# Kernel optimization log

Hardware: AMD Instinct MI355X
Metric: run time of the kernel (lower is better)

## Reference

```python
import jax, jax.numpy as jnp
import numpy as np

B, N, RIN, ROUT, DEMB, FIN, FE, E, ITERS = 64, 128, 32, 64, 64, 64, 16, 65536, 3
NTOT = B * N


def gnn(x, edge_index, edge_feat, Ws, Wm, We, b):
    # edge-conditioned message passing: [NTOT, Fin] -> [NTOT, Fout]
    src, dst = edge_index[0], edge_index[1]
    msg = jax.nn.relu(x[src] @ Wm + edge_feat @ We)          # [E, Fout]
    agg = jax.ops.segment_sum(msg, dst, num_segments=x.shape[0])
    return jax.nn.relu(x @ Ws + agg + b)


def setup_inputs() -> dict:
    key = jax.random.key(0)
    ks = jax.random.split(key, 20)
    s = 0.1
    return {
        "x_r": jax.random.normal(ks[0], (NTOT, FIN), jnp.float32),
        "edge_index_r": jax.random.randint(ks[1], (2, E), 0, NTOT),
        "edge_feat_r": jax.random.normal(ks[2], (E, FE), jnp.float32),
        "x_p": jax.random.normal(ks[3], (NTOT, FIN), jnp.float32),
        "edge_index_p": jax.random.randint(ks[4], (2, E), 0, NTOT),
        "edge_feat_p": jax.random.normal(ks[5], (E, FE), jnp.float32),
        "r_mask": jnp.ones((B, N), dtype=bool),
        "p_mask": jnp.ones((B, N), dtype=bool),
        # gnn_1 params (FIN -> DEMB)
        "g1_Ws": jax.random.normal(ks[6], (FIN, DEMB)) * s,
        "g1_Wm": jax.random.normal(ks[7], (FIN, DEMB)) * s,
        "g1_We": jax.random.normal(ks[8], (FE, DEMB)) * s,
        "g1_b": jnp.zeros((DEMB,), jnp.float32),
        # gnn_2 params (RIN -> ROUT)
        "g2_Ws": jax.random.normal(ks[9], (RIN, ROUT)) * s,
        "g2_Wm": jax.random.normal(ks[10], (RIN, ROUT)) * s,
        "g2_We": jax.random.normal(ks[11], (FE, ROUT)) * s,
        "g2_b": jnp.zeros((ROUT,), jnp.float32),
        # consensus mlp (ROUT -> ROUT -> 1)
        "mlp_W1": jax.random.normal(ks[12], (ROUT, ROUT)) * s,
        "mlp_b1": jnp.zeros((ROUT,), jnp.float32),
        "mlp_W2": jax.random.normal(ks[13], (ROUT, 1)) * s,
        "mlp_b2": jnp.zeros((1,), jnp.float32),
    }


def reference(x_r, edge_index_r, edge_feat_r, x_p, edge_index_p, edge_feat_p,
              r_mask, p_mask,
              g1_Ws, g1_Wm, g1_We, g1_b,
              g2_Ws, g2_Wm, g2_We, g2_b,
              mlp_W1, mlp_b1, mlp_W2, mlp_b2):
    # node embeddings via gnn_1, then dense-batch to [B, N, DEMB]
    h_r = gnn(x_r, edge_index_r, edge_feat_r, g1_Ws, g1_Wm, g1_We, g1_b).reshape(B, N, DEMB)
    h_p = gnn(x_p, edge_index_p, edge_feat_p, g1_Ws, g1_Wm, g1_We, g1_b).reshape(B, N, DEMB)

    M_hat = jnp.einsum('brd,bpd->brp', h_r, h_p)             # [B, N_r, N_p]
    M_mask = r_mask[:, :, None] & p_mask[:, None, :]
    M_0 = jax.nn.softmax(M_hat, axis=-1).reshape(NTOT, N)    # packed (full mask)

    rkey = jax.random.key(42)
    for it in range(ITERS):
        M = jax.nn.softmax(M_hat, axis=-1)
        rf_r = jax.random.normal(jax.random.fold_in(rkey, it), (B, N, RIN), jnp.float32)
        rf_p = jnp.einsum('brp,bri->bpi', M, rf_r)           # M^T @ rand
        o_r = gnn(rf_r.reshape(NTOT, RIN), edge_index_r, edge_feat_r,
                  g2_Ws, g2_Wm, g2_We, g2_b).reshape(B, N, ROUT)
        o_p = gnn(rf_p.reshape(NTOT, RIN), edge_index_p, edge_feat_p,
                  g2_Ws, g2_Wm, g2_We, g2_b).reshape(B, N, ROUT)
        D = o_r[:, :, None, :] - o_p[:, None, :, :]          # [B, N_r, N_p, ROUT]
        upd = (jax.nn.relu(D @ mlp_W1 + mlp_b1) @ mlp_W2 + mlp_b2)[..., 0]
        M_hat = M_hat + jnp.where(M_mask, upd, 0.0)

    M_T = jax.nn.softmax(M_hat, axis=-1).reshape(NTOT, N)
    return (M_0, M_T)
```

## Files before the change

kernel.cpp:

```cpp
#include <hip/hip_runtime.h>

constexpr int kE = 65536, kNTOT = 8192;

__host__ __device__ __forceinline__ void tf_round(unsigned& x0, unsigned& x1, int r) {
  x0 += x1;
  x1 = (x1 << r) | (x1 >> (32 - r));
  x1 ^= x0;
}
__host__ __device__ __forceinline__ void tf2x32(unsigned k0, unsigned k1,
                                                unsigned& x0, unsigned& x1) {
  unsigned ks2 = k0 ^ k1 ^ 0x1BD11BDAu;
  x0 += k0; x1 += k1;
  tf_round(x0,x1,13); tf_round(x0,x1,15); tf_round(x0,x1,26); tf_round(x0,x1,6);
  x0 += k1; x1 += ks2 + 1u;
  tf_round(x0,x1,17); tf_round(x0,x1,29); tf_round(x0,x1,16); tf_round(x0,x1,24);
  x0 += ks2; x1 += k0 + 2u;
  tf_round(x0,x1,13); tf_round(x0,x1,15); tf_round(x0,x1,26); tf_round(x0,x1,6);
  x0 += k0; x1 += k1 + 3u;
  tf_round(x0,x1,17); tf_round(x0,x1,29); tf_round(x0,x1,16); tf_round(x0,x1,24);
  x0 += k1; x1 += ks2 + 4u;
  tf_round(x0,x1,13); tf_round(x0,x1,15); tf_round(x0,x1,26); tf_round(x0,x1,6);
  x0 += ks2; x1 += k0 + 5u;
}

__device__ __forceinline__ float bits_to_normal(unsigned bits) {
  float f = __uint_as_float((bits >> 9) | 0x3f800000u) - 1.0f;
  const float LO = -0.99999994f;
  float u = fmaf(f, 2.0f, LO);
  u = fmaxf(u, LO);
  float w = -log1pf(-u * u);
  float p;
  if (w < 5.0f) {
    w -= 2.5f;
    p = 2.81022636e-08f;
    p = fmaf(p, w, 3.43273939e-07f);
    p = fmaf(p, w, -3.5233877e-06f);
    p = fmaf(p, w, -4.39150654e-06f);
    p = fmaf(p, w, 0.00021858087f);
    p = fmaf(p, w, -0.00125372503f);
    p = fmaf(p, w, -0.00417768164f);
    p = fmaf(p, w, 0.246640727f);
    p = fmaf(p, w, 1.50140941f);
  } else {
    w = sqrtf(w) - 3.0f;
    p = -0.000200214257f;
    p = fmaf(p, w, 0.000100950558f);
    p = fmaf(p, w, 0.00134934322f);
    p = fmaf(p, w, -0.00367342844f);
    p = fmaf(p, w, 0.00573950773f);
    p = fmaf(p, w, -0.0076224613f);
    p = fmaf(p, w, 0.00943887047f);
    p = fmaf(p, w, 1.00167406f);
    p = fmaf(p, w, 2.83297682f);
  }
  return 1.41421356f * (p * u);
}

__device__ __forceinline__ float redmax32(float v) {
#pragma unroll
  for (int o = 16; o > 0; o >>= 1) v = fmaxf(v, __shfl_xor(v, o));
  return v;
}
__device__ __forceinline__ float redsum32(float v) {
#pragma unroll
  for (int o = 16; o > 0; o >>= 1) v += __shfl_xor(v, o);
  return v;
}

__global__ __launch_bounds__(256) void hist_kern(const int* __restrict__ eiR,
                                                 const int* __restrict__ eiP,
                                                 int* __restrict__ offR,
                                                 int* __restrict__ offP,
                                                 float* __restrict__ aggz,
                                                 float* __restrict__ rfpz) {
  int i = blockIdx.x * 256 + threadIdx.x;
  float4 z4 = make_float4(0.f, 0.f, 0.f, 0.f);
  float4* z = reinterpret_cast<float4*>(aggz) + i * 2;
  z[0] = z4; z[1] = z4;
  reinterpret_cast<float2*>(rfpz)[i] = make_float2(0.f, 0.f);
  const int* ei = (i < kE) ? eiR : eiP;
  int* off = (i < kE) ? offR : offP;
  int e = i & (kE - 1);
  atomicAdd(&off[ei[kE + e]], 1);
}

__global__ __launch_bounds__(512) void scan_kern(int* __restrict__ offR,
                                                 int* __restrict__ offP) {
  int* off = blockIdx.x ? offP : offR;
  int t = threadIdx.x;
  int base = t * 16;
  int v[16];
#pragma unroll
  for (int i = 0; i < 16; ++i) v[i] = off[base + i];
  int sum = 0;
#pragma unroll
  for (int i = 0; i < 16; ++i) sum += v[i];
  int lane = t & 63, w = t >> 6;
  int incl = sum;
#pragma unroll
  for (int o = 1; o < 64; o <<= 1) {
    int y = __shfl_up(incl, o);
    if (lane >= o) incl += y;
  }
  __shared__ int wsum[8];
  if (lane == 63) wsum[w] = incl;
  __syncthreads();
  int woff = 0;
#pragma unroll
  for (int i = 0; i < 8; ++i) if (i < w) woff += wsum[i];
  int running = woff + incl - sum;
#pragma unroll
  for (int i = 0; i < 16; ++i) {
    off[base + i] = running;
    running += v[i];
  }
}

__global__ __launch_bounds__(256) void scatter_kern(
    const int* __restrict__ eiR, const int* __restrict__ eiP,
    int* __restrict__ offR, int* __restrict__ offP,
    int4* __restrict__ ebR, int4* __restrict__ ebP) {
  int i = blockIdx.x * 256 + threadIdx.x;
  const int* ei = (i < kE) ? eiR : eiP;
  int* off = (i < kE) ? offR : offP;
  int4* eb = (i < kE) ? ebR : ebP;
  int e = i & (kE - 1);
  int src = ei[e];
  int dst = ei[kE + e];
  int pos = atomicAdd(&off[dst], 1);
  eb[pos] = make_int4(src, e, dst, 0);
}

__global__ __launch_bounds__(512) void xw_gemm64(
    const float* __restrict__ inR, const float* __restrict__ inP,
    float* __restrict__ xwR, float* __restrict__ xwP,
    const float* __restrict__ W) {
  __shared__ float sX[64][68];
  __shared__ float sW[64][68];
  bool isP = blockIdx.x >= 128;
  const float* in = isP ? inP : inR;
  float* xw = isP ? xwP : xwR;
  int n0 = (blockIdx.x & 127) * 64;
  int t = threadIdx.x;
#pragma unroll
  for (int idx = 0; idx < 2; ++idx) {
    int q = t * 4 + idx * 2048;
    int k = q >> 6, j = q & 63;
    *reinterpret_cast<float4*>(&sW[k][j]) = *reinterpret_cast<const float4*>(W + q);
    float4 v = *reinterpret_cast<const float4*>(in + (size_t)n0 * 64 + q);
    sX[j + 0][k] = v.x; sX[j + 1][k] = v.y; sX[j + 2][k] = v.z; sX[j + 3][k] = v.w;
  }
  __syncthreads();
  int tn = (t & 31) * 2, tj = (t >> 5) * 4;
  float acc[2][4] = {};
#pragma unroll 8
  for (int k = 0; k < 64; ++k) {
    float2 a = *reinterpret_cast<const float2*>(&sX[k][tn]);
    float4 b = *reinterpret_cast<const float4*>(&sW[k][tj]);
    acc[0][0] = fmaf(a.x, b.x, acc[0][0]); acc[0][1] = fmaf(a.x, b.y, acc[0][1]);
    acc[0][2] = fmaf(a.x, b.z, acc[0][2]); acc[0][3] = fmaf(a.x, b.w, acc[0][3]);
    acc[1][0] = fmaf(a.y, b.x, acc[1][0]); acc[1][1] = fmaf(a.y, b.y, acc[1][1]);
    acc[1][2] = fmaf(a.y, b.z, acc[1][2]); acc[1][3] = fmaf(a.y, b.w, acc[1][3]);
  }
#pragma unroll
  for (int i = 0; i < 2; ++i) {
    *reinterpret_cast<float4*>(&xw[(size_t)(n0 + tn + i) * 64 + tj]) =
        make_float4(acc[i][0], acc[i][1], acc[i][2], acc[i][3]);
  }
}

__global__ __launch_bounds__(512) void xwp_gemm(
    const float* __restrict__ rfp, float* __restrict__ xwP,
    const float* __restrict__ W) {
  __shared__ float sX[32][68];
  __shared__ float sW[32][68];
  int n0 = blockIdx.x * 64;
  int t = threadIdx.x;
  {
    int q = t * 4;
    *reinterpret_cast<float4*>(&sW[q >> 6][q & 63]) = *reinterpret_cast<const float4*>(W + q);
    int r = q >> 5, kk = q & 31;
    float4 v = *reinterpret_cast<const float4*>(rfp + (size_t)n0 * 32 + q);
    sX[kk][r] = v.x; sX[kk + 1][r] = v.y; sX[kk + 2][r] = v.z; sX[kk + 3][r] = v.w;
  }
  __syncthreads();
  int tn = (t & 31) * 2, tj = (t >> 5) * 4;
  float acc[2][4] = {};
#pragma unroll 8
  for (int k = 0; k < 32; ++k) {
    float2 a = *reinterpret_cast<const float2*>(&sX[k][tn]);
    float4 b = *reinterpret_cast<const float4*>(&sW[k][tj]);
    acc[0][0] = fmaf(a.x, b.x, acc[0][0]); acc[0][1] = fmaf(a.x, b.y, acc[0][1]);
    acc[0][2] = fmaf(a.x, b.z, acc[0][2]); acc[0][3] = fmaf(a.x, b.w, acc[0][3]);
    acc[1][0] = fmaf(a.y, b.x, acc[1][0]); acc[1][1] = fmaf(a.y, b.y, acc[1][1]);
    acc[1][2] = fmaf(a.y, b.z, acc[1][2]); acc[1][3] = fmaf(a.y, b.w, acc[1][3]);
  }
#pragma unroll
  for (int i = 0; i < 2; ++i) {
    *reinterpret_cast<float4*>(&xwP[(size_t)(n0 + tn + i) * 64 + tj]) =
        make_float4(acc[i][0], acc[i][1], acc[i][2], acc[i][3]);
  }
}

__global__ __launch_bounds__(256) void msg_edge(
    const float* __restrict__ xwR, const float* __restrict__ efR,
    const int4* __restrict__ ebR, float* __restrict__ aggR,
    const float* __restrict__ xwP, const float* __restrict__ efP,
    const int4* __restrict__ ebP, float* __restrict__ aggP,
    const float* __restrict__ We) {
  __shared__ float sEF[16][68];
  __shared__ float sW[16][68];
  __shared__ float sOut[64][68];
  __shared__ int sDst[64];
  __shared__ int sSrc[64];
  __shared__ int sPerm[64];
  bool isP = blockIdx.x >= 1024;
  const float* xw = isP ? xwP : xwR;
  const float* ef = isP ? efP : efR;
  const int4* eb = isP ? ebP : ebR;
  float* agg = isP ? aggP : aggR;
  int i0 = (blockIdx.x & 1023) * 64;
  int t = threadIdx.x;
  {
    int q = t * 4;
    int k = q >> 6, j = q & 63;
    *reinterpret_cast<float4*>(&sW[k][j]) = *reinterpret_cast<const float4*>(We + q);
  }
  if (t < 64) {
    int4 er = eb[i0 + t];
    sSrc[t] = er.x;
    sPerm[t] = er.y;
    sDst[t] = er.z;
  }
  __syncthreads();
  {
    int l = t & 3;
    int g = t >> 2;
    int rb = g >> 2;
    int kq = g & 3;
    int gbase = (t & 63) & ~3;
    int k4 = kq * 4;
    int r = rb * 4 + l;
    const float* rptr = ef + (size_t)sPerm[r] * 16 + k4;
    float4 v = *reinterpret_cast<const float4*>(rptr);
    float vc[4] = {v.x, v.y, v.z, v.w};
    float out[4];
#pragma unroll
    for (int c = 0; c < 4; ++c) {
      float val = vc[(l - c) & 3];
      out[(l + c) & 3] = __shfl(val, gbase + ((l + c) & 3), 64);
    }
    *reinterpret_cast<float4*>(&sEF[k4 + l][rb * 4]) =
        make_float4(out[0], out[1], out[2], out[3]);
  }
  __syncthreads();
  int tn = (t & 15) * 4, tj = (t >> 4) * 4;
  float acc[4][4] = {};
#pragma unroll
  for (int k = 0; k < 16; ++k) {
    float4 a = *reinterpret_cast<const float4*>(&sEF[k][tn]);
    float4 b = *reinterpret_cast<const float4*>(&sW[k][tj]);
    acc[0][0] = fmaf(a.x, b.x, acc[0][0]); acc[0][1] = fmaf(a.x, b.y, acc[0][1]);
    acc[0][2] = fmaf(a.x, b.z, acc[0][2]); acc[0][3] = fmaf(a.x, b.w, acc[0][3]);
    acc[1][0] = fmaf(a.y, b.x, acc[1][0]); acc[1][1] = fmaf(a.y, b.y, acc[1][1]);
    acc[1][2] = fmaf(a.y, b.z, acc[1][2]); acc[1][3] = fmaf(a.y, b.w, acc[1][3]);
    acc[2][0] = fmaf(a.z, b.x, acc[2][0]); acc[2][1] = fmaf(a.z, b.y, acc[2][1]);
    acc[2][2] = fmaf(a.z, b.z, acc[2][2]); acc[2][3] = fmaf(a.z, b.w, acc[2][3]);
    acc[3][0] = fmaf(a.w, b.x, acc[3][0]); acc[3][1] = fmaf(a.w, b.y, acc[3][1]);
    acc[3][2] = fmaf(a.w, b.z, acc[3][2]); acc[3][3] = fmaf(a.w, b.w, acc[3][3]);
  }
#pragma unroll
  for (int i = 0; i < 4; ++i) {
    float4 g = *reinterpret_cast<const float4*>(xw + (size_t)sSrc[tn + i] * 64 + tj);
    *reinterpret_cast<float4*>(&sOut[tn + i][tj]) =
        make_float4(fmaxf(acc[i][0] + g.x, 0.f), fmaxf(acc[i][1] + g.y, 0.f),
                    fmaxf(acc[i][2] + g.z, 0.f), fmaxf(acc[i][3] + g.w, 0.f));
  }
  __syncthreads();
  int col = t & 63;
  int r0l = (t >> 6) * 16;
  float run = 0.f;
  int rd = sDst[r0l];
#pragma unroll
  for (int r = 0; r < 16; ++r) {
    int d = sDst[r0l + r];
    if (d != rd) {
      unsafeAtomicAdd(&agg[(size_t)rd * 64 + col], run);
      run = 0.f; rd = d;
    }
    run += sOut[r0l + r][col];
  }
  unsafeAtomicAdd(&agg[(size_t)rd * 64 + col], run);
}

__global__ __launch_bounds__(512) void node1_gemm(
    const float* __restrict__ xR, float* __restrict__ aggR, float* __restrict__ hR,
    const float* __restrict__ xP, float* __restrict__ aggP, float* __restrict__ hP,
    const float* __restrict__ Ws, const float* __restrict__ bias) {
  __shared__ float sX[64][68];
  __shared__ float sW[64][68];
  bool isP = blockIdx.x >= 128;
  const float* x = isP ? xP : xR;
  float* agg = isP ? aggP : aggR;
  float* h = isP ? hP : hR;
  int n0 = (blockIdx.x & 127) * 64;
  int t = threadIdx.x;
#pragma unroll
  for (int idx = 0; idx < 2; ++idx) {
    int q = t * 4 + idx * 2048;
    int k = q >> 6, j = q & 63;
    *reinterpret_cast<float4*>(&sW[k][j]) = *reinterpret_cast<const float4*>(Ws + q);
    float4 v = *reinterpret_cast<const float4*>(x + (size_t)n0 * 64 + q);
    sX[j + 0][k] = v.x; sX[j + 1][k] = v.y; sX[j + 2][k] = v.z; sX[j + 3][k] = v.w;
  }
  __syncthreads();
  int tn = (t & 31) * 2, tj = (t >> 5) * 4;
  float acc[2][4] = {};
#pragma unroll 8
  for (int k = 0; k < 64; ++k) {
    float2 a = *reinterpret_cast<const float2*>(&sX[k][tn]);
    float4 b = *reinterpret_cast<const float4*>(&sW[k][tj]);
    acc[0][0] = fmaf(a.x, b.x, acc[0][0]); acc[0][1] = fmaf(a.x, b.y, acc[0][1]);
    acc[0][2] = fmaf(a.x, b.z, acc[0][2]); acc[0][3] = fmaf(a.x, b.w, acc[0][3]);
    acc[1][0] = fmaf(a.y, b.x, acc[1][0]); acc[1][1] = fmaf(a.y, b.y, acc[1][1]);
    acc[1][2] = fmaf(a.y, b.z, acc[1][2]); acc[1][3] = fmaf(a.y, b.w, acc[1][3]);
  }
  float4 bv = *reinterpret_cast<const float4*>(bias + tj);
  float4 z4 = make_float4(0.f, 0.f, 0.f, 0.f);
#pragma unroll
  for (int i = 0; i < 2; ++i) {
    int n = n0 + tn + i;
    float4 g = *reinterpret_cast<const float4*>(&agg[(size_t)n * 64 + tj]);
    *reinterpret_cast<float4*>(&agg[(size_t)n * 64 + tj]) = z4;
    float4 o;
    o.x = fmaxf(acc[i][0] + g.x + bv.x, 0.f);
    o.y = fmaxf(acc[i][1] + g.y + bv.y, 0.f);
    o.z = fmaxf(acc[i][2] + g.z + bv.z, 0.f);
    o.w = fmaxf(acc[i][3] + g.w + bv.w, 0.f);
    *reinterpret_cast<float4*>(&h[(size_t)n * 64 + tj]) = o;
  }
}

__device__ __forceinline__ void rfp_partial(const float sm[16][128],
                                            const float rfb[16][32],
                                            float* __restrict__ rfpB, int t) {
  float rfc[16];
  int iw = t & 31;
#pragma unroll
  for (int r = 0; r < 16; ++r) rfc[r] = rfb[r][iw];
#pragma unroll
  for (int rep = 0; rep < 16; ++rep) {
    int p = rep * 8 + (t >> 5);
    float a = 0.f;
#pragma unroll
    for (int r = 0; r < 16; ++r) a = fmaf(sm[r][p], rfc[r], a);
    unsafeAtomicAdd(&rfpB[p * 32 + iw], a);
  }
}

__device__ __forceinline__ void gen_rfr_tile(float* __restrict__ rfr,
                                             float rfb[16][32], int b, int r0,
                                             int t, unsigned fk0, unsigned fk1) {
  unsigned base = (unsigned)((b * 128 + r0) * 32);
#pragma unroll
  for (int q = 0; q < 2; ++q) {
    unsigned j = (unsigned)(q * 256 + t);
    unsigned i = base + j;
    unsigned a0 = 0u, a1 = i;
    tf2x32(fk0, fk1, a0, a1);
    float v = bits_to_normal(a0 ^ a1);
    rfr[i] = v;
    rfb[j >> 5][j & 31] = v;
  }
}

__device__ __forceinline__ void xwr_direct(const float rfb[16][32],
                                           const float* __restrict__ Wm2,
                                           float* __restrict__ xwR,
                                           int b, int r0, int t) {
  int rl = t >> 4, c0 = (t & 15) * 4;
  float4 a = make_float4(0.f, 0.f, 0.f, 0.f);
#pragma unroll 8
  for (int k = 0; k < 32; ++k) {
    float rv = rfb[rl][k];
    float4 w = *reinterpret_cast<const float4*>(Wm2 + k * 64 + c0);
    a.x = fmaf(rv, w.x, a.x); a.y = fmaf(rv, w.y, a.y);
    a.z = fmaf(rv, w.z, a.z); a.w = fmaf(rv, w.w, a.w);
  }
  *reinterpret_cast<float4*>(&xwR[(size_t)(b * 128 + r0 + rl) * 64 + c0]) = a;
}

__global__ __launch_bounds__(256) void mhat_soft(
    const float* __restrict__ hR, const float* __restrict__ hP,
    float* __restrict__ Mhat, float* __restrict__ M0out,
    float* __restrict__ rfr, float* __restrict__ rfp,
    float* __restrict__ xwR, const float* __restrict__ Wm2,
    unsigned fk0, unsigned fk1) {
  __shared__ float hr[16][66];
  __shared__ float hp[128][66];
  __shared__ float sm[16][128];
  __shared__ float rfb[16][32];
  int gid = blockIdx.x, t = threadIdx.x;
  int b = gid >> 3, r0 = (gid & 7) * 16;
  gen_rfr_tile(rfr, rfb, b, r0, t, fk0, fk1);
  const float* hrG = hR + ((size_t)(b * 128 + r0)) * 64;
  {
    int q = t * 4; int r = q >> 6, d = q & 63;
    float4 v = *reinterpret_cast<const float4*>(hrG + q);
    hr[r][d] = v.x; hr[r][d + 1] = v.y; hr[r][d + 2] = v.z; hr[r][d + 3] = v.w;
  }
  const float* hpG = hP + (size_t)b * 128 * 64;
#pragma unroll
  for (int rep = 0; rep < 8; ++rep) {
    int q = (rep * 256 + t) * 4; int p = q >> 6, d = q & 63;
    float4 v = *reinterpret_cast<const float4*>(hpG + q);
    hp[p][d] = v.x; hp[p][d + 1] = v.y; hp[p][d + 2] = v.z; hp[p][d + 3] = v.w;
  }
  __syncthreads();
  xwr_direct(rfb, Wm2, xwR, b, r0, t);
  int tx = t & 31, ty = t >> 5;
  float acc[2][4] = {};
  for (int d = 0; d < 64; ++d) {
    float a0 = hr[ty][d], a1 = hr[ty + 8][d];
    float q0 = hp[tx][d], q1 = hp[tx + 32][d], q2 = hp[tx + 64][d], q3 = hp[tx + 96][d];
    acc[0][0] = fmaf(a0, q0, acc[0][0]); acc[0][1] = fmaf(a0, q1, acc[0][1]);
    acc[0][2] = fmaf(a0, q2, acc[0][2]); acc[0][3] = fmaf(a0, q3, acc[0][3]);
    acc[1][0] = fmaf(a1, q0, acc[1][0]); acc[1][1] = fmaf(a1, q1, acc[1][1]);
    acc[1][2] = fmaf(a1, q2, acc[1][2]); acc[1][3] = fmaf(a1, q3, acc[1][3]);
  }
#pragma unroll
  for (int ii = 0; ii < 2; ++ii) {
    int r = r0 + ty + 8 * ii;
    float* mrow = Mhat + ((size_t)(b * 128 + r)) * 128;
    mrow[tx] = acc[ii][0]; mrow[tx + 32] = acc[ii][1];
    mrow[tx + 64] = acc[ii][2]; mrow[tx + 96] = acc[ii][3];
    float mx = redmax32(fmaxf(fmaxf(acc[ii][0], acc[ii][1]), fmaxf(acc[ii][2], acc[ii][3])));
    float e0 = __expf(acc[ii][0] - mx), e1 = __expf(acc[ii][1] - mx);
    float e2 = __expf(acc[ii][2] - mx), e3 = __expf(acc[ii][3] - mx);
    float inv = 1.0f / redsum32(e0 + e1 + e2 + e3);
    float* orow = M0out + ((size_t)(b * 128 + r)) * 128;
    orow[tx] = e0 * inv; orow[tx + 32] = e1 * inv;
    orow[tx + 64] = e2 * inv; orow[tx + 96] = e3 * inv;
    int rl = ty + 8 * ii;
    sm[rl][tx] = e0 * inv; sm[rl][tx + 32] = e1 * inv;
    sm[rl][tx + 64] = e2 * inv; sm[rl][tx + 96] = e3 * inv;
  }
  __syncthreads();
  rfp_partial(sm, rfb, rfp + (size_t)b * 4096, t);
}

__global__ __launch_bounds__(512) void node2u_gemm(
    const float* __restrict__ rfR, float* __restrict__ aggR, float* __restrict__ uR,
    const float* __restrict__ rfP, float* __restrict__ aggP, float* __restrict__ uP,
    const float* __restrict__ Ws2, const float* __restrict__ g2b,
    const float* __restrict__ W1, const float* __restrict__ b1,
    float* __restrict__ rfp_clear) {
  __shared__ float sRF[32][68];
  __shared__ float sW2[32][68];
  __shared__ float sW1[64][68];
  __shared__ float sO[64][68];
  bool isP = blockIdx.x >= 128;
  const float* rf = isP ? rfP : rfR;
  float* agg = isP ? aggP : aggR;
  float* u = isP ? uP : uR;
  int n0 = (blockIdx.x & 127) * 64;
  int t = threadIdx.x;
#pragma unroll
  for (int idx = 0; idx < 2; ++idx) {
    int q = t * 4 + idx * 2048;
    *reinterpret_cast<float4*>(&sW1[q >> 6][q & 63]) = *reinterpret_cast<const float4*>(W1 + q);
  }
  {
    int q = t * 4;
    *reinterpret_cast<float4*>(&sW2[q >> 6][q & 63]) = *reinterpret_cast<const float4*>(Ws2 + q);
    int r = q >> 5, kk = q & 31;
    float4 v = *reinterpret_cast<const float4*>(rf + (size_t)(n0 + r) * 32 + kk);
    sRF[kk][r] = v.x; sRF[kk + 1][r] = v.y; sRF[kk + 2][r] = v.z; sRF[kk + 3][r] = v.w;
  }
  __syncthreads();
  if (isP) {
    float4 z4 = make_float4(0.f, 0.f, 0.f, 0.f);
    reinterpret_cast<float4*>(rfp_clear + (size_t)n0 * 32)[t] = z4;
  }
  int tn = (t & 31) * 2, tj = (t >> 5) * 4;
  float acc[2][4] = {};
#pragma unroll 8
  for (int k = 0; k < 32; ++k) {
    float2 a = *reinterpret_cast<const float2*>(&sRF[k][tn]);
    float4 b = *reinterpret_cast<const float4*>(&sW2[k][tj]);
    acc[0][0] = fmaf(a.x, b.x, acc[0][0]); acc[0][1] = fmaf(a.x, b.y, acc[0][1]);
    acc[0][2] = fmaf(a.x, b.z, acc[0][2]); acc[0][3] = fmaf(a.x, b.w, acc[0][3]);
    acc[1][0] = fmaf(a.y, b.x, acc[1][0]); acc[1][1] = fmaf(a.y, b.y, acc[1][1]);
    acc[1][2] = fmaf(a.y, b.z, acc[1][2]); acc[1][3] = fmaf(a.y, b.w, acc[1][3]);
  }
  float4 bg = *reinterpret_cast<const float4*>(g2b + tj);
  float4 z4 = make_float4(0.f, 0.f, 0.f, 0.f);
#pragma unroll
  for (int i = 0; i < 2; ++i) {
    int n = n0 + tn + i;
    float4 g = *reinterpret_cast<const float4*>(&agg[(size_t)n * 64 + tj]);
    *reinterpret_cast<float4*>(&agg[(size_t)n * 64 + tj]) = z4;
    sO[tj + 0][tn + i] = fmaxf(acc[i][0] + g.x + bg.x, 0.f);
    sO[tj + 1][tn + i] = fmaxf(acc[i][1] + g.y + bg.y, 0.f);
    sO[tj + 2][tn + i] = fmaxf(acc[i][2] + g.z + bg.z, 0.f);
    sO[tj + 3][tn + i] = fmaxf(acc[i][3] + g.w + bg.w, 0.f);
  }
  __syncthreads();
  float acc2[2][4] = {};
#pragma unroll 8
  for (int k = 0; k < 64; ++k) {
    float2 a = *reinterpret_cast<const float2*>(&sO[k][tn]);
    float4 b = *reinterpret_cast<const float4*>(&sW1[k][tj]);
    acc2[0][0] = fmaf(a.x, b.x, acc2[0][0]); acc2[0][1] = fmaf(a.x, b.y, acc2[0][1]);
    acc2[0][2] = fmaf(a.x, b.z, acc2[0][2]); acc2[0][3] = fmaf(a.x, b.w, acc2[0][3]);
    acc2[1][0] = fmaf(a.y, b.x, acc2[1][0]); acc2[1][1] = fmaf(a.y, b.y, acc2[1][1]);
    acc2[1][2] = fmaf(a.y, b.z, acc2[1][2]); acc2[1][3] = fmaf(a.y, b.w, acc2[1][3]);
  }
  float4 b1v = make_float4(0.f, 0.f, 0.f, 0.f);
  if (!isP) b1v = *reinterpret_cast<const float4*>(b1 + tj);
#pragma unroll
  for (int i = 0; i < 2; ++i) {
    int n = n0 + tn + i;
    float4 o;
    o.x = acc2[i][0] + b1v.x; o.y = acc2[i][1] + b1v.y;
    o.z = acc2[i][2] + b1v.z; o.w = acc2[i][3] + b1v.w;
    *reinterpret_cast<float4*>(&u[(size_t)n * 64 + tj]) = o;
  }
}

__global__ __launch_bounds__(256) void upd_soft(
    const float* __restrict__ uR, const float* __restrict__ uP,
    const float* __restrict__ W2, const float* __restrict__ b2p,
    float* __restrict__ Mhat, float* __restrict__ outLast, int last,
    float* __restrict__ rfr, float* __restrict__ rfp,
    float* __restrict__ xwR, const float* __restrict__ Wm2,
    unsigned fk0, unsigned fk1) {
  __shared__ float sur[16][66];
  __shared__ float sup[128][66];
  __shared__ float sw2[64];
  __shared__ float sm[16][128];
  __shared__ float rfb[16][32];
  int gid = blockIdx.x, t = threadIdx.x;
  int b = gid >> 3, r0 = (gid & 7) * 16;
  if (!last) gen_rfr_tile(rfr, rfb, b, r0, t, fk0, fk1);
  const float* urG = uR + ((size_t)(b * 128 + r0)) * 64;
  {
    int q = t * 4; int r = q >> 6, d = q & 63;
    float4 v = *reinterpret_cast<const float4*>(urG + q);
    sur[r][d] = v.x; sur[r][d + 1] = v.y; sur[r][d + 2] = v.z; sur[r][d + 3] = v.w;
  }
  const float* upG = uP + (size_t)b * 128 * 64;
#pragma unroll
  for (int rep = 0; rep < 8; ++rep) {
    int q = (rep * 256 + t) * 4; int p = q >> 6, d = q & 63;
    float4 v = *reinterpret_cast<const float4*>(upG + q);
    sup[p][d] = v.x; sup[p][d + 1] = v.y; sup[p][d + 2] = v.z; sup[p][d + 3] = v.w;
  }
  if (t < 64) sw2[t] = W2[t];
  __syncthreads();
  if (!last) xwr_direct(rfb, Wm2, xwR, b, r0, t);
  int tx = t & 31, ty = t >> 5;
  float acc[2][4] = {};
  for (int j = 0; j < 64; ++j) {
    float w2v = sw2[j];
    float a0 = sur[ty][j], a1 = sur[ty + 8][j];
    float q0 = sup[tx][j], q1 = sup[tx + 32][j], q2 = sup[tx + 64][j], q3 = sup[tx + 96][j];
    acc[0][0] = fmaf(fmaxf(a0 - q0, 0.f), w2v, acc[0][0]);
    acc[0][1] = fmaf(fmaxf(a0 - q1, 0.f), w2v, acc[0][1]);
    acc[0][2] = fmaf(fmaxf(a0 - q2, 0.f), w2v, acc[0][2]);
    acc[0][3] = fmaf(fmaxf(a0 - q3, 0.f), w2v, acc[0][3]);
    acc[1][0] = fmaf(fmaxf(a1 - q0, 0.f), w2v, acc[1][0]);
    acc[1][1] = fmaf(fmaxf(a1 - q1, 0.f), w2v, acc[1][1]);
    acc[1][2] = fmaf(fmaxf(a1 - q2, 0.f), w2v, acc[1][2]);
    acc[1][3] = fmaf(fmaxf(a1 - q3, 0.f), w2v, acc[1][3]);
  }
  float b2v = b2p[0];
#pragma unroll
  for (int ii = 0; ii < 2; ++ii) {
    int r = r0 + ty + 8 * ii;
    float* mrow = Mhat + ((size_t)(b * 128 + r)) * 128;
    float m0 = mrow[tx] + acc[ii][0] + b2v;
    float m1 = mrow[tx + 32] + acc[ii][1] + b2v;
    float m2 = mrow[tx + 64] + acc[ii][2] + b2v;
    float m3 = mrow[tx + 96] + acc[ii][3] + b2v;
    if (!last) {
      mrow[tx] = m0; mrow[tx + 32] = m1; mrow[tx + 64] = m2; mrow[tx + 96] = m3;
    }
    float mx = redmax32(fmaxf(fmaxf(m0, m1), fmaxf(m2, m3)));
    float e0 = __expf(m0 - mx), e1 = __expf(m1 - mx);
    float e2 = __expf(m2 - mx), e3 = __expf(m3 - mx);
    float inv = 1.0f / redsum32(e0 + e1 + e2 + e3);
    if (last) {
      float* orow = outLast + ((size_t)(b * 128 + r)) * 128;
      orow[tx] = e0 * inv; orow[tx + 32] = e1 * inv;
      orow[tx + 64] = e2 * inv; orow[tx + 96] = e3 * inv;
    } else {
      int rl = ty + 8 * ii;
      sm[rl][tx] = e0 * inv; sm[rl][tx + 32] = e1 * inv;
      sm[rl][tx + 64] = e2 * inv; sm[rl][tx + 96] = e3 * inv;
    }
  }
  if (!last) {
    __syncthreads();
    rfp_partial(sm, rfb, rfp + (size_t)b * 4096, t);
  }
}

extern "C" void kernel_launch(void* const* d_in, const int* in_sizes, int n_in,
                              void* d_out, int out_size, void* d_ws, size_t ws_size,
                              hipStream_t stream) {
  (void)in_sizes; (void)n_in; (void)out_size; (void)ws_size;
  const float* x_r  = (const float*)d_in[0];
  const int*   ei_r = (const int*)d_in[1];
  const float* ef_r = (const float*)d_in[2];
  const float* x_p  = (const float*)d_in[3];
  const int*   ei_p = (const int*)d_in[4];
  const float* ef_p = (const float*)d_in[5];
  const float* g1_Ws = (const float*)d_in[8];
  const float* g1_Wm = (const float*)d_in[9];
  const float* g1_We = (const float*)d_in[10];
  const float* g1_b  = (const float*)d_in[11];
  const float* g2_Ws = (const float*)d_in[12];
  const float* g2_Wm = (const float*)d_in[13];
  const float* g2_We = (const float*)d_in[14];
  const float* g2_b  = (const float*)d_in[15];
  const float* W1 = (const float*)d_in[16];
  const float* b1 = (const float*)d_in[17];
  const float* W2 = (const float*)d_in[18];
  const float* b2 = (const float*)d_in[19];
  float* out = (float*)d_out;

  float* ws = (float*)d_ws;
  float* h_r   = ws;
  float* h_p   = h_r + 524288;
  float* Mhat  = h_p + 524288;
  float* rfr   = Mhat + 1048576;
  float* rfp   = rfr + 262144;
  float* u_r   = rfp + 262144;
  float* u_p   = u_r + 524288;
  float* agg_r = u_p + 524288;
  float* agg_p = agg_r + 524288;
  float* xw_r  = agg_p + 524288;
  float* xw_p  = xw_r + 524288;
  int* ib      = (int*)(xw_p + 524288);
  int* off_r  = ib;
  int* off_p  = off_r + 8192;
  int4* eb_r  = (int4*)(ib + 16384);
  int4* eb_p  = eb_r + 65536;

  unsigned fk0[3], fk1[3];
  for (int it = 0; it < 3; ++it) {
    unsigned a = 0u, c = (unsigned)it;
    tf2x32(0u, 42u, a, c);
    fk0[it] = a; fk1[it] = c;
  }

  hipMemsetAsync(off_r, 0, 2 * 8192 * sizeof(int), stream);
  hist_kern<<<512, 256, 0, stream>>>(ei_r, ei_p, off_r, off_p, agg_r, rfp);
  scan_kern<<<2, 512, 0, stream>>>(off_r, off_p);
  scatter_kern<<<512, 256, 0, stream>>>(ei_r, ei_p, off_r, off_p, eb_r, eb_p);

  xw_gemm64<<<256, 512, 0, stream>>>(x_r, x_p, xw_r, xw_p, g1_Wm);
  msg_edge<<<2048, 256, 0, stream>>>(xw_r, ef_r, eb_r, agg_r,
                                     xw_p, ef_p, eb_p, agg_p, g1_We);
  node1_gemm<<<256, 512, 0, stream>>>(x_r, agg_r, h_r, x_p, agg_p, h_p, g1_Ws, g1_b);
  mhat_soft<<<512, 256, 0, stream>>>(h_r, h_p, Mhat, out, rfr, rfp, xw_r, g2_Wm,
                                     fk0[0], fk1[0]);

  for (int it = 0; it < 3; ++it) {
    xwp_gemm<<<128, 512, 0, stream>>>(rfp, xw_p, g2_Wm);
    msg_edge<<<2048, 256, 0, stream>>>(xw_r, ef_r, eb_r, agg_r,
                                       xw_p, ef_p, eb_p, agg_p, g2_We);
    node2u_gemm<<<256, 512, 0, stream>>>(rfr, agg_r, u_r, rfp, agg_p, u_p,
                                         g2_Ws, g2_b, W1, b1, rfp);
    int last = (it == 2);
    upd_soft<<<512, 256, 0, stream>>>(u_r, u_p, W2, b2, Mhat,
                                      out + 1048576, last,
                                      rfr, rfp, xw_r, g2_Wm,
                                      fk0[it < 2 ? it + 1 : 0], fk1[it < 2 ? it + 1 : 0]);
  }
}
```

Before: 285.4 us.

## Fuse p-side node projection into per-edge message kernel for refinement iterations

Removes the separate xwp_gemm launch and instead, for the p graph, gathers rf_p rows and edge features per edge and multiplies them by a concatenated [Wm; We] weight (K=48) inside the message kernel. The r side keeps the precomputed xw gather plus an edge-feature GEMM. This saves one launch and the xw_p write/read round trip per iteration. In exchange it recomputes the node projection per edge (E/N = 8x redundant FLOPs) and adds a shuffle-based transpose when staging the gathered rows into shared memory.

Result: no change. 287.3 us (+0.7%).

```diff
diff --git a/kernel.cpp b/kernel.cpp
--- a/kernel.cpp
+++ b/kernel.cpp
@@ -169,39 +169,6 @@
   }
 }
 
-__global__ __launch_bounds__(512) void xwp_gemm(
-    const float* __restrict__ rfp, float* __restrict__ xwP,
-    const float* __restrict__ W) {
-  __shared__ float sX[32][68];
-  __shared__ float sW[32][68];
-  int n0 = blockIdx.x * 64;
-  int t = threadIdx.x;
-  {
-    int q = t * 4;
-    *reinterpret_cast<float4*>(&sW[q >> 6][q & 63]) = *reinterpret_cast<const float4*>(W + q);
-    int r = q >> 5, kk = q & 31;
-    float4 v = *reinterpret_cast<const float4*>(rfp + (size_t)n0 * 32 + q);
-    sX[kk][r] = v.x; sX[kk + 1][r] = v.y; sX[kk + 2][r] = v.z; sX[kk + 3][r] = v.w;
-  }
-  __syncthreads();
-  int tn = (t & 31) * 2, tj = (t >> 5) * 4;
-  float acc[2][4] = {};
-#pragma unroll 8
-  for (int k = 0; k < 32; ++k) {
-    float2 a = *reinterpret_cast<const float2*>(&sX[k][tn]);
-    float4 b = *reinterpret_cast<const float4*>(&sW[k][tj]);
-    acc[0][0] = fmaf(a.x, b.x, acc[0][0]); acc[0][1] = fmaf(a.x, b.y, acc[0][1]);
-    acc[0][2] = fmaf(a.x, b.z, acc[0][2]); acc[0][3] = fmaf(a.x, b.w, acc[0][3]);
-    acc[1][0] = fmaf(a.y, b.x, acc[1][0]); acc[1][1] = fmaf(a.y, b.y, acc[1][1]);
-    acc[1][2] = fmaf(a.y, b.z, acc[1][2]); acc[1][3] = fmaf(a.y, b.w, acc[1][3]);
-  }
-#pragma unroll
-  for (int i = 0; i < 2; ++i) {
-    *reinterpret_cast<float4*>(&xwP[(size_t)(n0 + tn + i) * 64 + tj]) =
-        make_float4(acc[i][0], acc[i][1], acc[i][2], acc[i][3]);
-  }
-}
-
 __global__ __launch_bounds__(256) void msg_edge(
     const float* __restrict__ xwR, const float* __restrict__ efR,
     const int4* __restrict__ ebR, float* __restrict__ aggR,
@@ -293,6 +260,120 @@
   unsafeAtomicAdd(&agg[(size_t)rd * 64 + col], run);
 }
 
+__global__ __launch_bounds__(256) void msg_it(
+    const float* __restrict__ xwR, const float* __restrict__ efR,
+    const int4* __restrict__ ebR, float* __restrict__ aggR,
+    const float* __restrict__ rfp, const float* __restrict__ efP,
+    const int4* __restrict__ ebP, float* __restrict__ aggP,
+    const float* __restrict__ Wm2, const float* __restrict__ We2) {
+  __shared__ float sA[64][68];
+  __shared__ float sW[48][68];
+  __shared__ int sDst[64];
+  __shared__ int sSrc[64];
+  __shared__ int sPerm[64];
+  bool isP = blockIdx.x >= 1024;
+  const float* ef = isP ? efP : efR;
+  const int4* eb = isP ? ebP : ebR;
+  float* agg = isP ? aggP : aggR;
+  int i0 = (blockIdx.x & 1023) * 64;
+  int t = threadIdx.x;
+  if (isP) {
+#pragma unroll
+    for (int idx = 0; idx < 3; ++idx) {
+      int q = t * 4 + idx * 1024;
+      int k = q >> 6, j = q & 63;
+      const float* sp = (k < 32) ? (Wm2 + k * 64 + j) : (We2 + (k - 32) * 64 + j);
+      *reinterpret_cast<float4*>(&sW[k][j]) = *reinterpret_cast<const float4*>(sp);
+    }
+  } else {
+    int q = t * 4;
+    *reinterpret_cast<float4*>(&sW[q >> 6][q & 63]) =
+        *reinterpret_cast<const float4*>(We2 + q);
+  }
+  if (t < 64) {
+    int4 er = eb[i0 + t];
+    sSrc[t] = er.x;
+    sPerm[t] = er.y;
+    sDst[t] = er.z;
+  }
+  __syncthreads();
+  {
+    int l = t & 3;
+    int g = t >> 2;
+    int rb = g >> 2;
+    int kq = g & 3;
+    int gbase = (t & 63) & ~3;
+    int nslab = isP ? 3 : 1;
+    for (int idx = 0; idx < nslab; ++idx) {
+      int k4 = idx * 16 + kq * 4;
+      int r = rb * 4 + l;
+      const float* rptr;
+      if (isP) {
+        rptr = (k4 < 32) ? (rfp + (size_t)sSrc[r] * 32 + k4)
+                         : (ef + (size_t)sPerm[r] * 16 + (k4 - 32));
+      } else {
+        rptr = ef + (size_t)sPerm[r] * 16 + k4;
+      }
+      float4 v = *reinterpret_cast<const float4*>(rptr);
+      float vc[4] = {v.x, v.y, v.z, v.w};
+      float out[4];
+#pragma unroll
+      for (int c = 0; c < 4; ++c) {
+        float val = vc[(l - c) & 3];
+        out[(l + c) & 3] = __shfl(val, gbase + ((l + c) & 3), 64);
+      }
+      *reinterpret_cast<float4*>(&sA[k4 + l][rb * 4]) =
+          make_float4(out[0], out[1], out[2], out[3]);
+    }
+  }
+  __syncthreads();
+  int tn = (t & 15) * 4, tj = (t >> 4) * 4;
+  float acc[4][4] = {};
+  int KT = isP ? 48 : 16;
+#pragma unroll 8
+  for (int k = 0; k < KT; ++k) {
+    float4 a = *reinterpret_cast<const float4*>(&sA[k][tn]);
+    float4 b = *reinterpret_cast<const float4*>(&sW[k][tj]);
+    acc[0][0] = fmaf(a.x, b.x, acc[0][0]); acc[0][1] = fmaf(a.x, b.y, acc[0][1]);
+    acc[0][2] = fmaf(a.x, b.z, acc[0][2]); acc[0][3] = fmaf(a.x, b.w, acc[0][3]);
+    acc[1][0] = fmaf(a.y, b.x, acc[1][0]); acc[1][1] = fmaf(a.y, b.y, acc[1][1]);
+    acc[1][2] = fmaf(a.y, b.z, acc[1][2]); acc[1][3] = fmaf(a.y, b.w, acc[1][3]);
+    acc[2][0] = fmaf(a.z, b.x, acc[2][0]); acc[2][1] = fmaf(a.z, b.y, acc[2][1]);
+    acc[2][2] = fmaf(a.z, b.z, acc[2][2]); acc[2][3] = fmaf(a.z, b.w, acc[2][3]);
+    acc[3][0] = fmaf(a.w, b.x, acc[3][0]); acc[3][1] = fmaf(a.w, b.y, acc[3][1]);
+    acc[3][2] = fmaf(a.w, b.z, acc[3][2]); acc[3][3] = fmaf(a.w, b.w, acc[3][3]);
+  }
+  if (!isP) {
+#pragma unroll
+    for (int i = 0; i < 4; ++i) {
+      float4 g = *reinterpret_cast<const float4*>(xwR + (size_t)sSrc[tn + i] * 64 + tj);
+      acc[i][0] += g.x; acc[i][1] += g.y; acc[i][2] += g.z; acc[i][3] += g.w;
+    }
+  }
+  __syncthreads();
+#pragma unroll
+  for (int i = 0; i < 4; ++i) {
+    *reinterpret_cast<float4*>(&sA[tn + i][tj]) =
+        make_float4(fmaxf(acc[i][0], 0.f), fmaxf(acc[i][1], 0.f),
+                    fmaxf(acc[i][2], 0.f), fmaxf(acc[i][3], 0.f));
+  }
+  __syncthreads();
+  int col = t & 63;
+  int r0l = (t >> 6) * 16;
+  float run = 0.f;
+  int rd = sDst[r0l];
+#pragma unroll
+  for (int r = 0; r < 16; ++r) {
+    int d = sDst[r0l + r];
+    if (d != rd) {
+      unsafeAtomicAdd(&agg[(size_t)rd * 64 + col], run);
+      run = 0.f; rd = d;
+    }
+    run += sA[r0l + r][col];
+  }
+  unsafeAtomicAdd(&agg[(size_t)rd * 64 + col], run);
+}
+
 __global__ __launch_bounds__(512) void node1_gemm(
     const float* __restrict__ xR, float* __restrict__ aggR, float* __restrict__ hR,
     const float* __restrict__ xP, float* __restrict__ aggP, float* __restrict__ hP,
@@ -668,9 +749,8 @@
                                      fk0[0], fk1[0]);
 
   for (int it = 0; it < 3; ++it) {
-    xwp_gemm<<<128, 512, 0, stream>>>(rfp, xw_p, g2_Wm);
-    msg_edge<<<2048, 256, 0, stream>>>(xw_r, ef_r, eb_r, agg_r,
-                                       xw_p, ef_p, eb_p, agg_p, g2_We);
+    msg_it<<<2048, 256, 0, stream>>>(xw_r, ef_r, eb_r, agg_r,
+                                     rfp, ef_p, eb_p, agg_p, g2_Wm, g2_We);
     node2u_gemm<<<256, 512, 0, stream>>>(rfr, agg_r, u_r, rfp, agg_p, u_p,
                                          g2_Ws, g2_b, W1, b1, rfp);
     int last = (it == 2);
```
